# Kernel tuning notes

Measured on AMD Instinct MI355X. Metric: run time of the kernel, lower is better.

The kernel has to match this reference:

```python
import jax, jax.numpy as jnp
import numpy as np

N_NODES = 100000


def gcn_conv(x, edge_index, W, b):
    """PyG GCNConv: out = D^-1/2 (A+I) D^-1/2 (X W) + b, edge weights = 1."""
    n = x.shape[0]
    h = x @ W  # [N, F_out]
    row, col = edge_index[0], edge_index[1]  # source -> target
    ones = jnp.ones(row.shape[0], dtype=x.dtype)
    # degree on A + I (self loop contributes 1)
    deg = jax.ops.segment_sum(ones, col, num_segments=n) + 1.0
    dinv = jax.lax.rsqrt(deg)  # deg >= 1 so no inf
    norm = dinv[row] * dinv[col]  # [E]
    agg = jax.ops.segment_sum(h[row] * norm[:, None], col, num_segments=n)
    agg = agg + h * (dinv * dinv)[:, None]  # self-loop term
    return agg + b


def setup_inputs() -> dict:
    key = jax.random.key(0)
    ks = jax.random.split(key, 8)
    E = 3200000
    F_in, H, C = 128, 16, 2
    x = jax.random.normal(ks[0], (N_NODES, F_in), dtype=jnp.float32)
    edge_index = jax.random.randint(ks[1], (2, E), 0, N_NODES, dtype=jnp.int64)
    W1 = jax.random.normal(ks[2], (F_in, H), dtype=jnp.float32) * (1.0 / np.sqrt(F_in))
    b1 = jnp.zeros((H,), jnp.float32)
    W2 = jax.random.normal(ks[3], (H, H), dtype=jnp.float32) * (1.0 / np.sqrt(H))
    b2 = jnp.zeros((H,), jnp.float32)
    fc1_W = jax.random.normal(ks[4], (2 * H, H), dtype=jnp.float32) * (1.0 / np.sqrt(2 * H))
    fc1_b = jnp.zeros((H,), jnp.float32)
    fc2_W = jax.random.normal(ks[5], (H, C), dtype=jnp.float32) * (1.0 / np.sqrt(H))
    fc2_b = jnp.zeros((C,), jnp.float32)
    return {"x": x, "edge_index": edge_index, "W1": W1, "b1": b1, "W2": W2,
            "b2": b2, "fc1_W": fc1_W, "fc1_b": fc1_b, "fc2_W": fc2_W, "fc2_b": fc2_b}


def reference(x, edge_index, W1, b1, W2, b2, fc1_W, fc1_b, fc2_W, fc2_b):
    h = jax.nn.relu(gcn_conv(x, edge_index, W1, b1))
    h = jax.nn.relu(gcn_conv(h, edge_index, W2, b2))
    row, col = edge_index[0], edge_index[1]
    ef = jnp.concatenate([h[row], h[col]], axis=1)  # [E, 32]
    ef = jax.nn.relu(ef @ fc1_W + fc1_b)
    logits = ef @ fc2_W + fc2_b  # [E, 2]
    return jax.nn.log_softmax(logits, axis=1)
```

## Files before the change

### kernel.cpp

```cpp
#include <hip/hip_runtime.h>
#include <hip/hip_fp16.h>
#include <cstdint>
#include <cstddef>

#define F_IN 128
#define HID 16
#define NBUK 1024
#define NPB  128
#define CHUNK 8192

__global__ void k_detect(const int* __restrict__ eidx, int* __restrict__ flag) {
    if (blockIdx.x == 0 && threadIdx.x == 0) {
        int all0 = 1;
        for (int i = 0; i < 64; ++i) {
            if (eidx[2 * i + 1] != 0) { all0 = 0; break; }
        }
        *flag = all0;
    }
}

__device__ __forceinline__ int ld_idx(const int* __restrict__ p, int e, int is64) {
    return is64 ? p[2 * e] : p[e];
}

__launch_bounds__(256)
__global__ void k_bhist(const int* __restrict__ eidx, int E,
                        const int* __restrict__ flag, int* __restrict__ ghist) {
    __shared__ int lh[NBUK];
    int t = threadIdx.x;
    for (int i = t; i < NBUK; i += 256) lh[i] = 0;
    __syncthreads();
    int base = blockIdx.x * CHUNK;
    int cnt = min(CHUNK, E - base);
    int is64 = *flag;
    const int* colp = eidx + ((size_t)E << is64);
    for (int i = t; i < cnt; i += 256)
        atomicAdd(&lh[ld_idx(colp, base + i, is64) >> 7], 1);
    __syncthreads();
    for (int i = t; i < NBUK; i += 256)
        if (lh[i]) atomicAdd(&ghist[i], lh[i]);
}

__global__ void k_bscan(const int* __restrict__ ghist, int E,
                        int* __restrict__ boff, int* __restrict__ gcur) {
    __shared__ int s[NBUK];
    int t = threadIdx.x;
    int v = ghist[t];
    s[t] = v;
    __syncthreads();
    for (int off = 1; off < NBUK; off <<= 1) {
        int a = (t >= off) ? s[t - off] : 0;
        __syncthreads();
        s[t] += a;
        __syncthreads();
    }
    int excl = s[t] - v;
    boff[t] = excl;
    gcur[t] = excl;
    if (t == NBUK - 1) boff[NBUK] = E;
}

__launch_bounds__(256)
__global__ void k_bscatter(const int* __restrict__ eidx, int E,
                           const int* __restrict__ flag,
                           int* __restrict__ gcur, uint32_t* __restrict__ pairs) {
    __shared__ int lh[NBUK];
    __shared__ int lcur[NBUK];
    int t = threadIdx.x;
    for (int i = t; i < NBUK; i += 256) lh[i] = 0;
    __syncthreads();
    int base = blockIdx.x * CHUNK;
    int cnt = min(CHUNK, E - base);
    int is64 = *flag;
    const int* rowp = eidx;
    const int* colp = eidx + ((size_t)E << is64);
    for (int i = t; i < cnt; i += 256)
        atomicAdd(&lh[ld_idx(colp, base + i, is64) >> 7], 1);
    __syncthreads();
    for (int i = t; i < NBUK; i += 256) {
        int c = lh[i];
        lcur[i] = c ? atomicAdd(&gcur[i], c) : 0;
    }
    __syncthreads();
    for (int i = t; i < cnt; i += 256) {
        int c = ld_idx(colp, base + i, is64);
        int r = ld_idx(rowp, base + i, is64);
        int buk = c >> 7;
        int pos = atomicAdd(&lcur[buk], 1);
        pairs[pos] = (uint32_t)r | ((uint32_t)(c & 127) << 20);
    }
}

__launch_bounds__(256)
__global__ void k_bsort(const uint32_t* __restrict__ pairs, const int* __restrict__ boff,
                        int* __restrict__ srcs, int* __restrict__ noff,
                        float* __restrict__ dinv, int n) {
    __shared__ int cnt[NPB];
    __shared__ int scn[NPB];
    int t = threadIdx.x;
    int b = blockIdx.x;
    if (t < NPB) cnt[t] = 0;
    __syncthreads();
    int beg = boff[b], end = boff[b + 1];
    for (int k = beg + t; k < end; k += 256)
        atomicAdd(&cnt[pairs[k] >> 20], 1);
    __syncthreads();
    if (t < NPB) scn[t] = cnt[t];
    __syncthreads();
    for (int off = 1; off < NPB; off <<= 1) {
        int v = 0;
        if (t < NPB && t >= off) v = scn[t - off];
        __syncthreads();
        if (t < NPB) scn[t] += v;
        __syncthreads();
    }
    if (t < NPB) {
        int node = b * NPB + t;
        int excl = scn[t] - cnt[t];
        if (node <= n) noff[node] = beg + excl;
        if (node < n)  dinv[node] = rsqrtf((float)cnt[t] + 1.0f);
        cnt[t] = beg + excl;
    }
    __syncthreads();
    for (int k = beg + t; k < end; k += 256) {
        uint32_t p = pairs[k];
        int pos = atomicAdd(&cnt[p >> 20], 1);
        srcs[pos] = (int)(p & 0xFFFFF);
    }
}

__launch_bounds__(256)
__global__ void k_gemm1(const float* __restrict__ x, const float* __restrict__ W1,
                        const float* __restrict__ dinv, __half* __restrict__ hs, int n) {
    __shared__ float Wt[16 * 132];
    for (int i = threadIdx.x; i < F_IN * HID; i += 256) {
        int k = i >> 4, j = i & 15;
        Wt[j * 132 + k] = W1[i];
    }
    __syncthreads();
    int row = blockIdx.x * 16 + (threadIdx.x >> 4);
    int j = threadIdx.x & 15;
    if (row >= n) return;
    const float4* xr = (const float4*)(x + (size_t)row * F_IN);
    float acc = 0.f;
#pragma unroll
    for (int kk = 0; kk < 32; ++kk) {
        float4 xv = xr[kk];
        float4 wv = *(const float4*)&Wt[j * 132 + 4 * kk];
        acc += xv.x * wv.x + xv.y * wv.y + xv.z * wv.z + xv.w * wv.w;
    }
    hs[(size_t)row * HID + j] = __float2half(acc * dinv[row]);
}

template <int EPI>
__launch_bounds__(256)
__global__ void k_layer(const int* __restrict__ srcs, const int* __restrict__ noff,
                        const __half* __restrict__ hs, const float* __restrict__ dinv,
                        const float* __restrict__ bias, const float* __restrict__ Wnext,
                        __half* __restrict__ out0, __half* __restrict__ out1) {
    __shared__ float Ws[512];
    __shared__ float bs[16];
    __shared__ float srow[16 * 17];
    int t = threadIdx.x;
    int nw = (EPI == 0) ? 256 : 512;
    for (int i = t; i < nw; i += 256) Ws[i] = Wnext[i];
    if (t < 16) bs[t] = bias[t];
    __syncthreads();

    int i = blockIdx.x * 16 + (t >> 4);
    int j = t & 15;
    int beg = noff[i], end = noff[i + 1];
    float acc = __half2float(hs[(size_t)i * HID + j]);

    int kb = beg;
    for (; kb + 16 <= end; kb += 16) {
        int idx = srcs[kb + j];
#pragma unroll
        for (int m = 0; m < 16; ++m) {
            int r = __shfl(idx, m, 16);
            acc += __half2float(hs[(size_t)r * HID + j]);
        }
    }
    if (kb < end) {
        int lim = end - kb;
        int idx = srcs[kb + ((j < lim) ? j : (lim - 1))];
        for (int m = 0; m < lim; ++m) {
            int r = __shfl(idx, m, 16);
            acc += __half2float(hs[(size_t)r * HID + j]);
        }
    }

    float di = dinv[i];
    float hrelu = fmaxf(acc * di + bs[j], 0.f);
    int ln = t >> 4;
    __syncthreads();
    srow[ln * 17 + j] = hrelu;
    __syncthreads();
    float a0 = 0.f, a1 = 0.f;
#pragma unroll
    for (int k = 0; k < 16; ++k) {
        float hv = srow[ln * 17 + k];
        a0 += hv * Ws[k * 16 + j];
        if (EPI == 1) a1 += hv * Ws[(16 + k) * 16 + j];
    }
    if (EPI == 0) {
        out0[(size_t)i * HID + j] = __float2half(a0 * di);
    } else {
        out0[(size_t)i * HID + j] = __float2half(a0);
        out1[(size_t)i * HID + j] = __float2half(a1);
    }
}

__launch_bounds__(256)
__global__ void k_edge(const int* __restrict__ eidx, int E, const int* __restrict__ flag,
                       const __half* __restrict__ u, const __half* __restrict__ v,
                       const float* __restrict__ fc1b, const float* __restrict__ fc2W,
                       const float* __restrict__ fc2b, float* __restrict__ out) {
    __shared__ float b1s[16], W2s[32], b2s[2];
    if (threadIdx.x < 16) b1s[threadIdx.x] = fc1b[threadIdx.x];
    if (threadIdx.x < 32) W2s[threadIdx.x] = fc2W[threadIdx.x];
    if (threadIdx.x < 2) b2s[threadIdx.x] = fc2b[threadIdx.x];
    __syncthreads();
    int e = blockIdx.x * blockDim.x + threadIdx.x;
    if (e >= E) return;
    int is64 = *flag;
    const int* rowp = eidx;
    const int* colp = eidx + ((size_t)E << is64);
    int r = ld_idx(rowp, e, is64);
    int c = ld_idx(colp, e, is64);
    const uint4* up = (const uint4*)(u + (size_t)r * HID);
    const uint4* vp = (const uint4*)(v + (size_t)c * HID);
    uint4 U0 = up[0], U1 = up[1], V0 = vp[0], V1 = vp[1];
    float l0 = b2s[0], l1 = b2s[1];
#define PROC(uw, vw, jb)                                                        \
    {                                                                           \
        float2 fu = __half22float2(*(__half2*)&(uw));                           \
        float2 fv = __half22float2(*(__half2*)&(vw));                           \
        float z = fmaxf(fu.x + fv.x + b1s[jb], 0.f);                            \
        l0 += z * W2s[2 * (jb)]; l1 += z * W2s[2 * (jb) + 1];                   \
        z = fmaxf(fu.y + fv.y + b1s[(jb) + 1], 0.f);                            \
        l0 += z * W2s[2 * (jb) + 2]; l1 += z * W2s[2 * (jb) + 3];               \
    }
    PROC(U0.x, V0.x, 0) PROC(U0.y, V0.y, 2) PROC(U0.z, V0.z, 4) PROC(U0.w, V0.w, 6)
    PROC(U1.x, V1.x, 8) PROC(U1.y, V1.y, 10) PROC(U1.z, V1.z, 12) PROC(U1.w, V1.w, 14)
#undef PROC
    float m = fmaxf(l0, l1);
    float e0 = __expf(l0 - m), e1 = __expf(l1 - m);
    float lse = m + __logf(e0 + e1);
    ((float2*)out)[e] = make_float2(l0 - lse, l1 - lse);
}

static inline size_t rnd4(size_t v) { return (v + 3) & ~(size_t)3; }

extern "C" void kernel_launch(void* const* d_in, const int* in_sizes, int n_in,
                              void* d_out, int out_size, void* d_ws, size_t ws_size,
                              hipStream_t stream) {
    const float* x    = (const float*)d_in[0];
    const int*   eidx = (const int*)d_in[1];
    const float* W1   = (const float*)d_in[2];
    const float* b1   = (const float*)d_in[3];
    const float* W2   = (const float*)d_in[4];
    const float* b2   = (const float*)d_in[5];
    const float* fc1W = (const float*)d_in[6];
    const float* fc1b = (const float*)d_in[7];
    const float* fc2W = (const float*)d_in[8];
    const float* fc2b = (const float*)d_in[9];

    const int n = in_sizes[0] / F_IN;
    const int E = in_sizes[1] / 2;
    const int NBLK_SORT = (E + CHUNK - 1) / CHUNK;
    const int NBLK_BUK  = (n + NPB - 1) / NPB;

    float* ws = (float*)d_ws;
    size_t a = 0;
    float*    dinv  = ws + a;              a += rnd4(n);
    uint32_t* pairs = (uint32_t*)(ws + a); a += rnd4(E);
    int*      srcs  = (int*)(ws + a);      a += rnd4(E);
    int*      noff  = (int*)(ws + a);      a += rnd4(n + 1);
    int*      boff  = (int*)(ws + a);      a += rnd4(NBUK + 1);
    int*      gcur  = (int*)(ws + a);      a += NBUK;
    int*      ghist = (int*)(ws + a);      a += NBUK;
    int*      flag  = (int*)(ws + a);      a += 4;
    __half*   hs1   = (__half*)(ws + a);   a += rnd4((size_t)n * HID / 2);
    __half*   hs2   = (__half*)(ws + a);   a += rnd4((size_t)n * HID / 2);
    __half*   ubuf  = (__half*)(ws + a);   a += rnd4((size_t)n * HID / 2);
    __half*   vbuf  = (__half*)(ws + a);   a += rnd4((size_t)n * HID / 2);
    float* out = (float*)d_out;

    k_detect<<<1, 64, 0, stream>>>(eidx, flag);

    hipMemsetAsync(ghist, 0, NBUK * sizeof(int), stream);
    k_bhist<<<NBLK_SORT, 256, 0, stream>>>(eidx, E, flag, ghist);
    k_bscan<<<1, NBUK, 0, stream>>>(ghist, E, boff, gcur);
    k_bscatter<<<NBLK_SORT, 256, 0, stream>>>(eidx, E, flag, gcur, pairs);
    k_bsort<<<NBLK_BUK, 256, 0, stream>>>(pairs, boff, srcs, noff, dinv, n);

    k_gemm1<<<(n + 15) / 16, 256, 0, stream>>>(x, W1, dinv, hs1, n);

    k_layer<0><<<n / 16, 256, 0, stream>>>(srcs, noff, hs1, dinv, b1, W2, hs2, nullptr);
    k_layer<1><<<n / 16, 256, 0, stream>>>(srcs, noff, hs2, dinv, b2, fc1W, ubuf, vbuf);
    k_edge<<<(E + 255) / 256, 256, 0, stream>>>(eidx, E, flag, ubuf, vbuf,
                                                fc1b, fc2W, fc2b, out);
}
```

Baseline: 271.5 us.

## Move fc1 projection into edge kernel, coarsen sort buckets, add nontemporal loads

The fc1 linear layer no longer runs per node to produce u/v buffers. The edge kernel now gathers h2 rows for both endpoints and computes the 32x16 matvec itself, handling two edges per thread. This removes one node-level pass and shrinks gathered data to a single buffer, but adds about 512 FMAs per edge. The bucket sort now uses 256 buckets of 512 nodes, so k_bsort runs with 512 threads, and nontemporal loads and stores are added across the index streams, x and the output.

New measurement: 571.9 us. 111% more time.

```diff
diff --git a/kernel.cpp b/kernel.cpp
--- a/kernel.cpp
+++ b/kernel.cpp
@@ -5,9 +5,11 @@
 
 #define F_IN 128
 #define HID 16
-#define NBUK 1024
-#define NPB  128
+#define NBUK 256
+#define NPB  512
 #define CHUNK 8192
+
+typedef float f4v __attribute__((ext_vector_type(4)));
 
 __global__ void k_detect(const int* __restrict__ eidx, int* __restrict__ flag) {
     if (blockIdx.x == 0 && threadIdx.x == 0) {
@@ -22,23 +24,26 @@
 __device__ __forceinline__ int ld_idx(const int* __restrict__ p, int e, int is64) {
     return is64 ? p[2 * e] : p[e];
 }
+__device__ __forceinline__ int ld_idx_nt(const int* __restrict__ p, int e, int is64) {
+    return is64 ? __builtin_nontemporal_load(&p[2 * e])
+                : __builtin_nontemporal_load(&p[e]);
+}
 
 __launch_bounds__(256)
 __global__ void k_bhist(const int* __restrict__ eidx, int E,
                         const int* __restrict__ flag, int* __restrict__ ghist) {
     __shared__ int lh[NBUK];
     int t = threadIdx.x;
-    for (int i = t; i < NBUK; i += 256) lh[i] = 0;
+    if (t < NBUK) lh[t] = 0;
     __syncthreads();
     int base = blockIdx.x * CHUNK;
     int cnt = min(CHUNK, E - base);
     int is64 = *flag;
     const int* colp = eidx + ((size_t)E << is64);
     for (int i = t; i < cnt; i += 256)
-        atomicAdd(&lh[ld_idx(colp, base + i, is64) >> 7], 1);
-    __syncthreads();
-    for (int i = t; i < NBUK; i += 256)
-        if (lh[i]) atomicAdd(&ghist[i], lh[i]);
+        atomicAdd(&lh[ld_idx_nt(colp, base + i, is64) >> 9], 1);
+    __syncthreads();
+    if (t < NBUK && lh[t]) atomicAdd(&ghist[t], lh[t]);
 }
 
 __global__ void k_bscan(const int* __restrict__ ghist, int E,
@@ -67,7 +72,7 @@
     __shared__ int lh[NBUK];
     __shared__ int lcur[NBUK];
     int t = threadIdx.x;
-    for (int i = t; i < NBUK; i += 256) lh[i] = 0;
+    if (t < NBUK) lh[t] = 0;
     __syncthreads();
     int base = blockIdx.x * CHUNK;
     int cnt = min(CHUNK, E - base);
@@ -75,23 +80,23 @@
     const int* rowp = eidx;
     const int* colp = eidx + ((size_t)E << is64);
     for (int i = t; i < cnt; i += 256)
-        atomicAdd(&lh[ld_idx(colp, base + i, is64) >> 7], 1);
-    __syncthreads();
-    for (int i = t; i < NBUK; i += 256) {
-        int c = lh[i];
-        lcur[i] = c ? atomicAdd(&gcur[i], c) : 0;
+        atomicAdd(&lh[ld_idx_nt(colp, base + i, is64) >> 9], 1);
+    __syncthreads();
+    if (t < NBUK) {
+        int c = lh[t];
+        lcur[t] = c ? atomicAdd(&gcur[t], c) : 0;
     }
     __syncthreads();
     for (int i = t; i < cnt; i += 256) {
-        int c = ld_idx(colp, base + i, is64);
-        int r = ld_idx(rowp, base + i, is64);
-        int buk = c >> 7;
+        int c = ld_idx_nt(colp, base + i, is64);
+        int r = ld_idx_nt(rowp, base + i, is64);
+        int buk = c >> 9;
         int pos = atomicAdd(&lcur[buk], 1);
-        pairs[pos] = (uint32_t)r | ((uint32_t)(c & 127) << 20);
-    }
-}
-
-__launch_bounds__(256)
+        pairs[pos] = (uint32_t)r | ((uint32_t)(c & (NPB - 1)) << 20);
+    }
+}
+
+__launch_bounds__(512)
 __global__ void k_bsort(const uint32_t* __restrict__ pairs, const int* __restrict__ boff,
                         int* __restrict__ srcs, int* __restrict__ noff,
                         float* __restrict__ dinv, int n) {
@@ -99,30 +104,27 @@
     __shared__ int scn[NPB];
     int t = threadIdx.x;
     int b = blockIdx.x;
-    if (t < NPB) cnt[t] = 0;
+    cnt[t] = 0;
     __syncthreads();
     int beg = boff[b], end = boff[b + 1];
-    for (int k = beg + t; k < end; k += 256)
+    for (int k = beg + t; k < end; k += 512)
         atomicAdd(&cnt[pairs[k] >> 20], 1);
     __syncthreads();
-    if (t < NPB) scn[t] = cnt[t];
+    scn[t] = cnt[t];
     __syncthreads();
     for (int off = 1; off < NPB; off <<= 1) {
-        int v = 0;
-        if (t < NPB && t >= off) v = scn[t - off];
+        int v = (t >= off) ? scn[t - off] : 0;
         __syncthreads();
-        if (t < NPB) scn[t] += v;
+        scn[t] += v;
         __syncthreads();
     }
-    if (t < NPB) {
-        int node = b * NPB + t;
-        int excl = scn[t] - cnt[t];
-        if (node <= n) noff[node] = beg + excl;
-        if (node < n)  dinv[node] = rsqrtf((float)cnt[t] + 1.0f);
-        cnt[t] = beg + excl;
-    }
-    __syncthreads();
-    for (int k = beg + t; k < end; k += 256) {
+    int node = b * NPB + t;
+    int excl = scn[t] - cnt[t];
+    if (node <= n) noff[node] = beg + excl;
+    if (node < n)  dinv[node] = rsqrtf((float)cnt[t] + 1.0f);
+    cnt[t] = beg + excl;
+    __syncthreads();
+    for (int k = beg + t; k < end; k += 512) {
         uint32_t p = pairs[k];
         int pos = atomicAdd(&cnt[p >> 20], 1);
         srcs[pos] = (int)(p & 0xFFFFF);
@@ -141,11 +143,11 @@
     int row = blockIdx.x * 16 + (threadIdx.x >> 4);
     int j = threadIdx.x & 15;
     if (row >= n) return;
-    const float4* xr = (const float4*)(x + (size_t)row * F_IN);
+    const f4v* xr = (const f4v*)(x + (size_t)row * F_IN);
     float acc = 0.f;
 #pragma unroll
     for (int kk = 0; kk < 32; ++kk) {
-        float4 xv = xr[kk];
+        f4v xv = __builtin_nontemporal_load(&xr[kk]);
         float4 wv = *(const float4*)&Wt[j * 132 + 4 * kk];
         acc += xv.x * wv.x + xv.y * wv.y + xv.z * wv.z + xv.w * wv.w;
     }
@@ -157,13 +159,12 @@
 __global__ void k_layer(const int* __restrict__ srcs, const int* __restrict__ noff,
                         const __half* __restrict__ hs, const float* __restrict__ dinv,
                         const float* __restrict__ bias, const float* __restrict__ Wnext,
-                        __half* __restrict__ out0, __half* __restrict__ out1) {
-    __shared__ float Ws[512];
+                        __half* __restrict__ out0) {
+    __shared__ float Ws[256];
     __shared__ float bs[16];
     __shared__ float srow[16 * 17];
     int t = threadIdx.x;
-    int nw = (EPI == 0) ? 256 : 512;
-    for (int i = t; i < nw; i += 256) Ws[i] = Wnext[i];
+    if (EPI == 0) { if (t < 256) Ws[t] = Wnext[t]; }
     if (t < 16) bs[t] = bias[t];
     __syncthreads();
 
@@ -174,7 +175,7 @@
 
     int kb = beg;
     for (; kb + 16 <= end; kb += 16) {
-        int idx = srcs[kb + j];
+        int idx = __builtin_nontemporal_load(&srcs[kb + j]);
 #pragma unroll
         for (int m = 0; m < 16; ++m) {
             int r = __shfl(idx, m, 16);
@@ -192,62 +193,98 @@
 
     float di = dinv[i];
     float hrelu = fmaxf(acc * di + bs[j], 0.f);
+    if (EPI == 1) {
+        out0[(size_t)i * HID + j] = __float2half(hrelu);
+        return;
+    }
     int ln = t >> 4;
-    __syncthreads();
     srow[ln * 17 + j] = hrelu;
     __syncthreads();
-    float a0 = 0.f, a1 = 0.f;
-#pragma unroll
-    for (int k = 0; k < 16; ++k) {
-        float hv = srow[ln * 17 + k];
-        a0 += hv * Ws[k * 16 + j];
-        if (EPI == 1) a1 += hv * Ws[(16 + k) * 16 + j];
-    }
-    if (EPI == 0) {
-        out0[(size_t)i * HID + j] = __float2half(a0 * di);
-    } else {
-        out0[(size_t)i * HID + j] = __float2half(a0);
-        out1[(size_t)i * HID + j] = __float2half(a1);
-    }
+    float a0 = 0.f;
+#pragma unroll
+    for (int k = 0; k < 16; ++k) a0 += srow[ln * 17 + k] * Ws[k * 16 + j];
+    out0[(size_t)i * HID + j] = __float2half(a0 * di);
 }
 
 __launch_bounds__(256)
 __global__ void k_edge(const int* __restrict__ eidx, int E, const int* __restrict__ flag,
-                       const __half* __restrict__ u, const __half* __restrict__ v,
+                       const __half* __restrict__ h2, const float* __restrict__ fc1W,
                        const float* __restrict__ fc1b, const float* __restrict__ fc2W,
                        const float* __restrict__ fc2b, float* __restrict__ out) {
-    __shared__ float b1s[16], W2s[32], b2s[2];
-    if (threadIdx.x < 16) b1s[threadIdx.x] = fc1b[threadIdx.x];
-    if (threadIdx.x < 32) W2s[threadIdx.x] = fc2W[threadIdx.x];
-    if (threadIdx.x < 2) b2s[threadIdx.x] = fc2b[threadIdx.x];
-    __syncthreads();
-    int e = blockIdx.x * blockDim.x + threadIdx.x;
-    if (e >= E) return;
+    __shared__ float2 WS[256];
+    __shared__ float2 b1s[8];
+    __shared__ float W2s[32], b2s[2];
+    int t = threadIdx.x;
+    WS[t] = ((const float2*)fc1W)[t];
+    if (t < 8)  b1s[t] = ((const float2*)fc1b)[t];
+    if (t < 32) W2s[t] = fc2W[t];
+    if (t < 2)  b2s[t] = fc2b[t];
+    __syncthreads();
+
+    int Eh = (E + 1) >> 1;
+    int e0 = blockIdx.x * 256 + t;
+    if (e0 >= Eh) return;
+    int e1 = e0 + Eh;
+    bool has1 = (e1 < E);
     int is64 = *flag;
     const int* rowp = eidx;
     const int* colp = eidx + ((size_t)E << is64);
-    int r = ld_idx(rowp, e, is64);
-    int c = ld_idx(colp, e, is64);
-    const uint4* up = (const uint4*)(u + (size_t)r * HID);
-    const uint4* vp = (const uint4*)(v + (size_t)c * HID);
-    uint4 U0 = up[0], U1 = up[1], V0 = vp[0], V1 = vp[1];
-    float l0 = b2s[0], l1 = b2s[1];
-#define PROC(uw, vw, jb)                                                        \
-    {                                                                           \
-        float2 fu = __half22float2(*(__half2*)&(uw));                           \
-        float2 fv = __half22float2(*(__half2*)&(vw));                           \
-        float z = fmaxf(fu.x + fv.x + b1s[jb], 0.f);                            \
-        l0 += z * W2s[2 * (jb)]; l1 += z * W2s[2 * (jb) + 1];                   \
-        z = fmaxf(fu.y + fv.y + b1s[(jb) + 1], 0.f);                            \
-        l0 += z * W2s[2 * (jb) + 2]; l1 += z * W2s[2 * (jb) + 3];               \
-    }
-    PROC(U0.x, V0.x, 0) PROC(U0.y, V0.y, 2) PROC(U0.z, V0.z, 4) PROC(U0.w, V0.w, 6)
-    PROC(U1.x, V1.x, 8) PROC(U1.y, V1.y, 10) PROC(U1.z, V1.z, 12) PROC(U1.w, V1.w, 14)
-#undef PROC
-    float m = fmaxf(l0, l1);
-    float e0 = __expf(l0 - m), e1 = __expf(l1 - m);
-    float lse = m + __logf(e0 + e1);
-    ((float2*)out)[e] = make_float2(l0 - lse, l1 - lse);
+    int r0 = ld_idx_nt(rowp, e0, is64), c0 = ld_idx_nt(colp, e0, is64);
+    int r1 = has1 ? ld_idx_nt(rowp, e1, is64) : r0;
+    int c1 = has1 ? ld_idx_nt(colp, e1, is64) : c0;
+
+    const uint4* p;
+    p = (const uint4*)(h2 + (size_t)r0 * HID); uint4 A0 = p[0], A1 = p[1];
+    p = (const uint4*)(h2 + (size_t)c0 * HID); uint4 B0 = p[0], B1 = p[1];
+    p = (const uint4*)(h2 + (size_t)r1 * HID); uint4 C0 = p[0], C1 = p[1];
+    p = (const uint4*)(h2 + (size_t)c1 * HID); uint4 D0 = p[0], D1 = p[1];
+
+    float fr0[16], fc0[16], fr1[16], fc1v[16];
+#define UNP(dst, X, Y) { float2 u_;                                         \
+    u_ = __half22float2(*(__half2*)&X.x); dst[0] = u_.x; dst[1] = u_.y;     \
+    u_ = __half22float2(*(__half2*)&X.y); dst[2] = u_.x; dst[3] = u_.y;     \
+    u_ = __half22float2(*(__half2*)&X.z); dst[4] = u_.x; dst[5] = u_.y;     \
+    u_ = __half22float2(*(__half2*)&X.w); dst[6] = u_.x; dst[7] = u_.y;     \
+    u_ = __half22float2(*(__half2*)&Y.x); dst[8] = u_.x; dst[9] = u_.y;     \
+    u_ = __half22float2(*(__half2*)&Y.y); dst[10] = u_.x; dst[11] = u_.y;   \
+    u_ = __half22float2(*(__half2*)&Y.z); dst[12] = u_.x; dst[13] = u_.y;   \
+    u_ = __half22float2(*(__half2*)&Y.w); dst[14] = u_.x; dst[15] = u_.y; }
+    UNP(fr0, A0, A1) UNP(fc0, B0, B1) UNP(fr1, C0, C1) UNP(fc1v, D0, D1)
+#undef UNP
+
+    float2 z0[8], z1[8];
+#pragma unroll
+    for (int m = 0; m < 8; ++m) { z0[m] = b1s[m]; z1[m] = b1s[m]; }
+#pragma unroll
+    for (int k = 0; k < 16; ++k) {
+        float ar0 = fr0[k], ac0 = fc0[k], ar1 = fr1[k], ac1 = fc1v[k];
+#pragma unroll
+        for (int m = 0; m < 8; ++m) {
+            float2 wa = WS[k * 8 + m], wb = WS[128 + k * 8 + m];
+            z0[m].x += ar0 * wa.x + ac0 * wb.x;
+            z0[m].y += ar0 * wa.y + ac0 * wb.y;
+            z1[m].x += ar1 * wa.x + ac1 * wb.x;
+            z1[m].y += ar1 * wa.y + ac1 * wb.y;
+        }
+    }
+
+#define FIN(zarr, ee) {                                                     \
+    float l0 = b2s[0], l1 = b2s[1];                                         \
+    _Pragma("unroll")                                                       \
+    for (int m = 0; m < 8; ++m) {                                           \
+        float zx = fmaxf(zarr[m].x, 0.f), zy = fmaxf(zarr[m].y, 0.f);       \
+        l0 += zx * W2s[4 * m]     + zy * W2s[4 * m + 2];                    \
+        l1 += zx * W2s[4 * m + 1] + zy * W2s[4 * m + 3];                    \
+    }                                                                       \
+    float mm = fmaxf(l0, l1);                                               \
+    float ex0 = __expf(l0 - mm), ex1 = __expf(l1 - mm);                     \
+    float lse = mm + __logf(ex0 + ex1);                                     \
+    float* op = out + 2 * (size_t)(ee);                                     \
+    __builtin_nontemporal_store(l0 - lse, op);                              \
+    __builtin_nontemporal_store(l1 - lse, op + 1); }
+    FIN(z0, e0)
+    if (has1) FIN(z1, e1)
+#undef FIN
 }
 
 static inline size_t rnd4(size_t v) { return (v + 3) & ~(size_t)3; }
@@ -283,8 +320,7 @@
     int*      flag  = (int*)(ws + a);      a += 4;
     __half*   hs1   = (__half*)(ws + a);   a += rnd4((size_t)n * HID / 2);
     __half*   hs2   = (__half*)(ws + a);   a += rnd4((size_t)n * HID / 2);
-    __half*   ubuf  = (__half*)(ws + a);   a += rnd4((size_t)n * HID / 2);
-    __half*   vbuf  = (__half*)(ws + a);   a += rnd4((size_t)n * HID / 2);
+    __half*   h2b   = (__half*)(ws + a);   a += rnd4((size_t)n * HID / 2);
     float* out = (float*)d_out;
 
     k_detect<<<1, 64, 0, stream>>>(eidx, flag);
@@ -293,12 +329,15 @@
     k_bhist<<<NBLK_SORT, 256, 0, stream>>>(eidx, E, flag, ghist);
     k_bscan<<<1, NBUK, 0, stream>>>(ghist, E, boff, gcur);
     k_bscatter<<<NBLK_SORT, 256, 0, stream>>>(eidx, E, flag, gcur, pairs);
-    k_bsort<<<NBLK_BUK, 256, 0, stream>>>(pairs, boff, srcs, noff, dinv, n);
+    k_bsort<<<NBLK_BUK, 512, 0, stream>>>(pairs, boff, srcs, noff, dinv, n);
 
     k_gemm1<<<(n + 15) / 16, 256, 0, stream>>>(x, W1, dinv, hs1, n);
 
-    k_layer<0><<<n / 16, 256, 0, stream>>>(srcs, noff, hs1, dinv, b1, W2, hs2, nullptr);
-    k_layer<1><<<n / 16, 256, 0, stream>>>(srcs, noff, hs2, dinv, b2, fc1W, ubuf, vbuf);
-    k_edge<<<(E + 255) / 256, 256, 0, stream>>>(eidx, E, flag, ubuf, vbuf,
-                                                fc1b, fc2W, fc2b, out);
-}
+    k_layer<0><<<n / 16, 256, 0, stream>>>(srcs, noff, hs1, dinv, b1, W2, hs2);
+    k_layer<1><<<n / 16, 256, 0, stream>>>(srcs, noff, hs2, dinv, b2, nullptr, h2b);
+    {
+        int Eh = (E + 1) >> 1;
+        k_edge<<<(Eh + 255) / 256, 256, 0, stream>>>(eidx, E, flag, h2b,
+                                                     fc1W, fc1b, fc2W, fc2b, out);
+    }
+}
```

## Add nontemporal loads, two edges per thread, larger scatter blocks, drop a barrier

Applied to the files above, without the earlier changes.

Streaming reads of the edge indices, x and srcs now use nontemporal loads, so single-use data is less likely to displace the reused node features in cache. The edge MLP kernel handles two edges per thread, with vectorized index loads and a single vectorized nontemporal store, to raise memory-level parallelism. The bucket-scatter kernel now uses 512-thread blocks over 16K-edge chunks, which halves the global cursor atomics. A redundant barrier before the shared-row write in the layer kernel is removed. The risks are lower occupancy from the extra registers in the edge kernel and the cache hints being ignored or counterproductive.

Measured after the change: 315.7 us. 16.3% more time.

```diff
diff --git a/kernel.cpp b/kernel.cpp
--- a/kernel.cpp
+++ b/kernel.cpp
@@ -8,6 +8,12 @@
 #define NBUK 1024
 #define NPB  128
 #define CHUNK 8192
+#define CHUNK2 16384
+
+typedef float f4v __attribute__((ext_vector_type(4)));
+typedef float f2v __attribute__((ext_vector_type(2)));
+typedef int   i2v __attribute__((ext_vector_type(2)));
+typedef int   i4v __attribute__((ext_vector_type(4)));
 
 __global__ void k_detect(const int* __restrict__ eidx, int* __restrict__ flag) {
     if (blockIdx.x == 0 && threadIdx.x == 0) {
@@ -19,8 +25,9 @@
     }
 }
 
-__device__ __forceinline__ int ld_idx(const int* __restrict__ p, int e, int is64) {
-    return is64 ? p[2 * e] : p[e];
+__device__ __forceinline__ int ld_idx_nt(const int* __restrict__ p, int e, int is64) {
+    return is64 ? __builtin_nontemporal_load(&p[2 * e])
+                : __builtin_nontemporal_load(&p[e]);
 }
 
 __launch_bounds__(256)
@@ -35,7 +42,7 @@
     int is64 = *flag;
     const int* colp = eidx + ((size_t)E << is64);
     for (int i = t; i < cnt; i += 256)
-        atomicAdd(&lh[ld_idx(colp, base + i, is64) >> 7], 1);
+        atomicAdd(&lh[ld_idx_nt(colp, base + i, is64) >> 7], 1);
     __syncthreads();
     for (int i = t; i < NBUK; i += 256)
         if (lh[i]) atomicAdd(&ghist[i], lh[i]);
@@ -60,34 +67,35 @@
     if (t == NBUK - 1) boff[NBUK] = E;
 }
 
-__launch_bounds__(256)
+__launch_bounds__(512)
 __global__ void k_bscatter(const int* __restrict__ eidx, int E,
                            const int* __restrict__ flag,
                            int* __restrict__ gcur, uint32_t* __restrict__ pairs) {
     __shared__ int lh[NBUK];
     __shared__ int lcur[NBUK];
     int t = threadIdx.x;
-    for (int i = t; i < NBUK; i += 256) lh[i] = 0;
-    __syncthreads();
-    int base = blockIdx.x * CHUNK;
-    int cnt = min(CHUNK, E - base);
+    for (int i = t; i < NBUK; i += 512) lh[i] = 0;
+    __syncthreads();
+    int base = blockIdx.x * CHUNK2;
+    int cnt = min(CHUNK2, E - base);
     int is64 = *flag;
     const int* rowp = eidx;
     const int* colp = eidx + ((size_t)E << is64);
-    for (int i = t; i < cnt; i += 256)
-        atomicAdd(&lh[ld_idx(colp, base + i, is64) >> 7], 1);
-    __syncthreads();
-    for (int i = t; i < NBUK; i += 256) {
+    for (int i = t; i < cnt; i += 512)
+        atomicAdd(&lh[ld_idx_nt(colp, base + i, is64) >> 7], 1);
+    __syncthreads();
+    for (int i = t; i < NBUK; i += 512) {
         int c = lh[i];
         lcur[i] = c ? atomicAdd(&gcur[i], c) : 0;
     }
     __syncthreads();
-    for (int i = t; i < cnt; i += 256) {
-        int c = ld_idx(colp, base + i, is64);
-        int r = ld_idx(rowp, base + i, is64);
+    for (int i = t; i < cnt; i += 512) {
+        int e = base + i;
+        int c = ld_idx_nt(colp, e, is64);
+        int r = ld_idx_nt(rowp, e, is64);
         int buk = c >> 7;
         int pos = atomicAdd(&lcur[buk], 1);
-        pairs[pos] = (uint32_t)r | ((uint32_t)(c & 127) << 20);
+        pairs[pos] = (uint32_t)r | ((uint32_t)(c & (NPB - 1)) << 20);
     }
 }
 
@@ -141,11 +149,11 @@
     int row = blockIdx.x * 16 + (threadIdx.x >> 4);
     int j = threadIdx.x & 15;
     if (row >= n) return;
-    const float4* xr = (const float4*)(x + (size_t)row * F_IN);
+    const f4v* xr = (const f4v*)(x + (size_t)row * F_IN);
     float acc = 0.f;
 #pragma unroll
     for (int kk = 0; kk < 32; ++kk) {
-        float4 xv = xr[kk];
+        f4v xv = __builtin_nontemporal_load(&xr[kk]);
         float4 wv = *(const float4*)&Wt[j * 132 + 4 * kk];
         acc += xv.x * wv.x + xv.y * wv.y + xv.z * wv.z + xv.w * wv.w;
     }
@@ -174,7 +182,7 @@
 
     int kb = beg;
     for (; kb + 16 <= end; kb += 16) {
-        int idx = srcs[kb + j];
+        int idx = __builtin_nontemporal_load(&srcs[kb + j]);
 #pragma unroll
         for (int m = 0; m < 16; ++m) {
             int r = __shfl(idx, m, 16);
@@ -193,7 +201,6 @@
     float di = dinv[i];
     float hrelu = fmaxf(acc * di + bs[j], 0.f);
     int ln = t >> 4;
-    __syncthreads();
     srow[ln * 17 + j] = hrelu;
     __syncthreads();
     float a0 = 0.f, a1 = 0.f;
@@ -212,7 +219,8 @@
 }
 
 __launch_bounds__(256)
-__global__ void k_edge(const int* __restrict__ eidx, int E, const int* __restrict__ flag,
+__global__ void k_edge(const int* __restrict__ eidx, int E,
+                       const int* __restrict__ flag,
                        const __half* __restrict__ u, const __half* __restrict__ v,
                        const float* __restrict__ fc1b, const float* __restrict__ fc2W,
                        const float* __restrict__ fc2b, float* __restrict__ out) {
@@ -221,18 +229,32 @@
     if (threadIdx.x < 32) W2s[threadIdx.x] = fc2W[threadIdx.x];
     if (threadIdx.x < 2) b2s[threadIdx.x] = fc2b[threadIdx.x];
     __syncthreads();
-    int e = blockIdx.x * blockDim.x + threadIdx.x;
-    if (e >= E) return;
+    int g = blockIdx.x * blockDim.x + threadIdx.x;
+    int e0 = 2 * g;
+    if (e0 >= E) return;
+    bool has1 = (e0 + 1 < E);
     int is64 = *flag;
     const int* rowp = eidx;
     const int* colp = eidx + ((size_t)E << is64);
-    int r = ld_idx(rowp, e, is64);
-    int c = ld_idx(colp, e, is64);
-    const uint4* up = (const uint4*)(u + (size_t)r * HID);
-    const uint4* vp = (const uint4*)(v + (size_t)c * HID);
-    uint4 U0 = up[0], U1 = up[1], V0 = vp[0], V1 = vp[1];
-    float l0 = b2s[0], l1 = b2s[1];
-#define PROC(uw, vw, jb)                                                        \
+    int r0, c0, r1, c1;
+    if (is64) {
+        i4v rw = __builtin_nontemporal_load((const i4v*)(rowp + 2 * (size_t)e0));
+        i4v cw = __builtin_nontemporal_load((const i4v*)(colp + 2 * (size_t)e0));
+        r0 = rw.x; r1 = rw.z; c0 = cw.x; c1 = cw.z;
+    } else {
+        i2v rw = __builtin_nontemporal_load((const i2v*)(rowp + e0));
+        i2v cw = __builtin_nontemporal_load((const i2v*)(colp + e0));
+        r0 = rw.x; r1 = rw.y; c0 = cw.x; c1 = cw.y;
+    }
+    if (!has1) { r1 = r0; c1 = c0; }
+    const uint4* p0 = (const uint4*)(u + (size_t)r0 * HID);
+    const uint4* q0 = (const uint4*)(v + (size_t)c0 * HID);
+    const uint4* p1 = (const uint4*)(u + (size_t)r1 * HID);
+    const uint4* q1 = (const uint4*)(v + (size_t)c1 * HID);
+    uint4 U0a = p0[0], U0b = p0[1], V0a = q0[0], V0b = q0[1];
+    uint4 U1a = p1[0], U1b = p1[1], V1a = q1[0], V1b = q1[1];
+
+#define PROC(l0, l1, uw, vw, jb)                                                \
     {                                                                           \
         float2 fu = __half22float2(*(__half2*)&(uw));                           \
         float2 fv = __half22float2(*(__half2*)&(vw));                           \
@@ -241,13 +263,29 @@
         z = fmaxf(fu.y + fv.y + b1s[(jb) + 1], 0.f);                            \
         l0 += z * W2s[2 * (jb) + 2]; l1 += z * W2s[2 * (jb) + 3];               \
     }
-    PROC(U0.x, V0.x, 0) PROC(U0.y, V0.y, 2) PROC(U0.z, V0.z, 4) PROC(U0.w, V0.w, 6)
-    PROC(U1.x, V1.x, 8) PROC(U1.y, V1.y, 10) PROC(U1.z, V1.z, 12) PROC(U1.w, V1.w, 14)
+    float a0 = b2s[0], a1 = b2s[1];
+    PROC(a0, a1, U0a.x, V0a.x, 0) PROC(a0, a1, U0a.y, V0a.y, 2)
+    PROC(a0, a1, U0a.z, V0a.z, 4) PROC(a0, a1, U0a.w, V0a.w, 6)
+    PROC(a0, a1, U0b.x, V0b.x, 8) PROC(a0, a1, U0b.y, V0b.y, 10)
+    PROC(a0, a1, U0b.z, V0b.z, 12) PROC(a0, a1, U0b.w, V0b.w, 14)
+    float b0 = b2s[0], b1v = b2s[1];
+    PROC(b0, b1v, U1a.x, V1a.x, 0) PROC(b0, b1v, U1a.y, V1a.y, 2)
+    PROC(b0, b1v, U1a.z, V1a.z, 4) PROC(b0, b1v, U1a.w, V1a.w, 6)
+    PROC(b0, b1v, U1b.x, V1b.x, 8) PROC(b0, b1v, U1b.y, V1b.y, 10)
+    PROC(b0, b1v, U1b.z, V1b.z, 12) PROC(b0, b1v, U1b.w, V1b.w, 14)
 #undef PROC
-    float m = fmaxf(l0, l1);
-    float e0 = __expf(l0 - m), e1 = __expf(l1 - m);
-    float lse = m + __logf(e0 + e1);
-    ((float2*)out)[e] = make_float2(l0 - lse, l1 - lse);
+    float m0 = fmaxf(a0, a1);
+    float lse0 = m0 + __logf(__expf(a0 - m0) + __expf(a1 - m0));
+    float m1 = fmaxf(b0, b1v);
+    float lse1 = m1 + __logf(__expf(b0 - m1) + __expf(b1v - m1));
+    if (has1) {
+        f4v res; res.x = a0 - lse0; res.y = a1 - lse0;
+        res.z = b0 - lse1; res.w = b1v - lse1;
+        __builtin_nontemporal_store(res, (f4v*)(out + 2 * (size_t)e0));
+    } else {
+        f2v res; res.x = a0 - lse0; res.y = a1 - lse0;
+        __builtin_nontemporal_store(res, (f2v*)(out + 2 * (size_t)e0));
+    }
 }
 
 static inline size_t rnd4(size_t v) { return (v + 3) & ~(size_t)3; }
@@ -268,7 +306,8 @@
 
     const int n = in_sizes[0] / F_IN;
     const int E = in_sizes[1] / 2;
-    const int NBLK_SORT = (E + CHUNK - 1) / CHUNK;
+    const int NBLK_HIST = (E + CHUNK - 1) / CHUNK;
+    const int NBLK_SCAT = (E + CHUNK2 - 1) / CHUNK2;
     const int NBLK_BUK  = (n + NPB - 1) / NPB;
 
     float* ws = (float*)d_ws;
@@ -289,16 +328,19 @@
 
     k_detect<<<1, 64, 0, stream>>>(eidx, flag);
 
-    hipMemsetAsync(ghist, 0, NBUK * sizeof(int), stream);
-    k_bhist<<<NBLK_SORT, 256, 0, stream>>>(eidx, E, flag, ghist);
+    (void)hipMemsetAsync(ghist, 0, NBUK * sizeof(int), stream);
+    k_bhist<<<NBLK_HIST, 256, 0, stream>>>(eidx, E, flag, ghist);
     k_bscan<<<1, NBUK, 0, stream>>>(ghist, E, boff, gcur);
-    k_bscatter<<<NBLK_SORT, 256, 0, stream>>>(eidx, E, flag, gcur, pairs);
+    k_bscatter<<<NBLK_SCAT, 512, 0, stream>>>(eidx, E, flag, gcur, pairs);
     k_bsort<<<NBLK_BUK, 256, 0, stream>>>(pairs, boff, srcs, noff, dinv, n);
 
     k_gemm1<<<(n + 15) / 16, 256, 0, stream>>>(x, W1, dinv, hs1, n);
 
     k_layer<0><<<n / 16, 256, 0, stream>>>(srcs, noff, hs1, dinv, b1, W2, hs2, nullptr);
     k_layer<1><<<n / 16, 256, 0, stream>>>(srcs, noff, hs2, dinv, b2, fc1W, ubuf, vbuf);
-    k_edge<<<(E + 255) / 256, 256, 0, stream>>>(eidx, E, flag, ubuf, vbuf,
-                                                fc1b, fc2W, fc2b, out);
-}
+    {
+        int npair = (E + 1) / 2;
+        k_edge<<<(npair + 255) / 256, 256, 0, stream>>>(eidx, E, flag, ubuf, vbuf,
+                                                        fc1b, fc2W, fc2b, out);
+    }
+}
```
